# Performance work log

Hardware: AMD Instinct MI355X
Metric: run time of the kernel (lower is better)

## Reference

```python
import jax, jax.numpy as jnp
import numpy as np

N = 12288   # nodes
E = 393216  # edges (avg degree 32)
B = 16      # graphs in batch
F_IN = 15   # node feature dim
H = 32      # hidden_dim
EMB = 64    # embedding_dim
NC = 11     # num_classes
EDIM = 2    # edge feature dim
EPS = 1e-5  # BatchNorm eps


def _bn(x, gamma, beta):
    # training-mode BatchNorm1d: biased batch variance, matches torch normalization
    mu = jnp.mean(x, axis=0)
    var = jnp.var(x, axis=0)
    return gamma * (x - mu) * jax.lax.rsqrt(var + EPS) + beta


def setup_inputs() -> dict:
    key = jax.random.key(0)
    ks = jax.random.split(key, 16)
    def p(k, shape, s=0.05):
        return jax.random.normal(k, shape, dtype=jnp.float32) * s
    z = lambda *s: jnp.zeros(s, jnp.float32)
    o = lambda *s: jnp.ones(s, jnp.float32)
    return {
        "x": jax.random.normal(ks[0], (N, F_IN), dtype=jnp.float32),
        "edge_attr": jax.random.normal(ks[1], (E, EDIM), dtype=jnp.float32),
        "w_edge": p(ks[2], (EDIM, 1)), "b_edge": z(1),
        "w1": p(ks[3], (F_IN, H)), "b1": z(H), "g1": o(H), "be1": z(H),
        "w2": p(ks[4], (H, 2 * H)), "b2": z(2 * H), "g2": o(2 * H), "be2": z(2 * H),
        "w3": p(ks[5], (2 * H, EMB)), "b3": z(EMB), "g3": o(EMB), "be3": z(EMB),
        "wf1": p(ks[6], (EMB, 512)), "bf1": z(512), "gf1": o(512), "bef1": z(512),
        "wf2": p(ks[7], (512, 256)), "bf2": z(256), "gf2": o(256), "bef2": z(256),
        "wf3": p(ks[8], (256, NC)), "bf3": z(NC),
        "edge_index": jax.random.randint(ks[9], (2, E), 0, N, dtype=jnp.int64)
                      if jax.config.jax_enable_x64 else jax.random.randint(ks[9], (2, E), 0, N),
        "batch": jnp.sort(jax.random.randint(ks[10], (N,), 0, B)),
    }


def reference(x, edge_attr, w_edge, b_edge,
              w1, b1, g1, be1, w2, b2, g2, be2, w3, b3, g3, be3,
              wf1, bf1, gf1, bef1, wf2, bf2, gf2, bef2, wf3, bf3,
              edge_index, batch):
    # edge weights: sigmoid(Linear(edge_attr)) -> [E]
    ew = jax.nn.sigmoid(edge_attr @ w_edge + b_edge)[:, 0]
    # dense adjacency with self loops, accumulate duplicates (sparse_coo.to_dense)
    loop = jnp.arange(N)
    row = jnp.concatenate([edge_index[0], loop])
    col = jnp.concatenate([edge_index[1], loop])
    w_aug = jnp.concatenate([ew, jnp.ones((N,), ew.dtype)])
    adj = jnp.zeros((N, N), ew.dtype).at[row, col].add(w_aug)
    # symmetric degree normalization D^-1/2 A D^-1/2
    deg = adj.sum(axis=1)
    dis = jnp.where(deg > 0, jax.lax.rsqrt(jnp.where(deg > 0, deg, 1.0)), 0.0)
    support = dis[:, None] * adj * dis[None, :]
    # three GCN layers: support @ x @ W + b, BN, relu
    h = jax.nn.relu(_bn(support @ x @ w1 + b1, g1, be1))
    h = jax.nn.relu(_bn(support @ h @ w2 + b2, g2, be2))
    h = jax.nn.relu(_bn(support @ h @ w3 + b3, g3, be3))
    # global max pool per graph (empty graphs -> zeros)
    seg = jax.ops.segment_max(h, batch, num_segments=B)
    cnt = jax.ops.segment_sum(jnp.ones((N,), h.dtype), batch, num_segments=B)
    emb = jnp.where(cnt[:, None] > 0, seg, 0.0)
    # MLP head (dropout = identity at inference)
    o = jax.nn.relu(_bn(emb @ wf1 + bf1, gf1, bef1))
    o = jax.nn.relu(_bn(o @ wf2 + bf2, gf2, bef2))
    logits = o @ wf3 + bf3
    return jax.nn.log_softmax(logits, axis=1), emb
```

## Files before the change

### kernel.cpp

```cpp
#include <hip/hip_runtime.h>

#define NN   12288
#define EE   393216
#define WELL 128
#define NELL (NN*WELL)
#define BG   16
#define FIN  15
#define FH1  32
#define FH2  64
#define NCL  11
#define BNEPS 1e-5f
#define NBANK 32

typedef unsigned long long u64;
static inline int cdiv(long a, long b){ return (int)((a + b - 1) / b); }

__device__ __forceinline__ int getIdx(const void* p, long i, int is64){
  return is64 ? (int)((const long long*)p)[i] : ((const int*)p)[i];
}

__device__ __forceinline__ float degOf(unsigned lo){
  return 1.0f + (float)lo * (1.0f/1048576.0f);
}

__global__ void k_pre(u64* deg_cnt, float* csp1, float* csp2, float* csp3,
                      float* embf, const void* ei, const void* batch, int* flags){
  int g = blockIdx.x*256 + threadIdx.x;
  if (g < NN) deg_cnt[g] = 0ull;
  if (g < NBANK*128){ csp1[g] = 0.f; csp2[g] = 0.f; csp3[g] = 0.f; }
  if (g < BG*64) embf[g] = 0.f;
  if (blockIdx.x == 0 && threadIdx.x < 64){
    const int* a = (const int*)ei;
    unsigned long long m0 = __ballot(a[2*threadIdx.x + 1] == 0);
    const int* b = (const int*)batch;
    int j = 96*threadIdx.x;
    unsigned long long m1 = __ballot(b[2*j + 1] == 0);
    if (threadIdx.x == 0){
      flags[0] = (m0 == ~0ull) ? 1 : 0;
      flags[1] = (m1 == ~0ull) ? 1 : 0;
    }
  }
}

__global__ void k_edge(const float* ea, const float* we, const float* bedg,
                       const void* ei, const int* flags, u64* deg_cnt,
                       unsigned* csr_p){
  int e = blockIdx.x*256 + threadIdx.x;
  if (e >= EE) return;
  int is64 = flags[0];
  float2 eav = ((const float2*)ea)[e];
  float z = eav.x*we[0] + eav.y*we[1] + bedg[0];
  float w = 1.0f/(1.0f + expf(-z));
  int r = getIdx(ei, e, is64);
  int c = getIdx(ei, (long)EE + e, is64);
  u64 add = (1ull << 32) | (u64)__float2uint_rn(w * 1048576.0f);
  u64 old = atomicAdd(&deg_cnt[r], add);
  int slot = (int)(old >> 32);
  if (slot < WELL){
    unsigned wfix = __float2uint_rn(w * 131072.0f);
    csr_p[((long)r << 7) + slot] = (unsigned)c | (wfix << 14);
  }
}

__global__ void __launch_bounds__(256) k_fix2(const u64* __restrict__ deg_cnt,
                                              unsigned* __restrict__ csr_p){
  int row = blockIdx.x*4 + (threadIdx.x >> 6);
  int lane = threadIdx.x & 63;
  const unsigned* cl = (const unsigned*)deg_cnt;
  int n = (int)(deg_cnt[row] >> 32);
  n = n < WELL ? n : WELL;
  for (int s = lane; s < n; s += 64){
    long idx = ((long)row << 7) + s;
    unsigned v = csr_p[idx];
    int c = (int)(v & 16383u);
    float w = (float)(v >> 14) * (1.0f/131072.0f);
    w *= rsqrtf(degOf(cl[2*c]));
    csr_p[idx] = (unsigned)c | (__float2uint_rn(w * 131072.0f) << 14);
  }
}

template<int F, int FP, int FO, int APPLY_BN>
__global__ void __launch_bounds__(256) k_layer(
    const float* __restrict__ Hin,
    const float* __restrict__ cspin, const float* __restrict__ gam,
    const float* __restrict__ bet,
    const float* __restrict__ W, const float* __restrict__ bias,
    const u64* __restrict__ deg_cnt, const unsigned* __restrict__ csr_p,
    float* __restrict__ Pout, float* __restrict__ csout){
  const int R2 = 256/(FP*2);
  __shared__ float At[R2][FP];
  __shared__ float Apart[256];
  __shared__ float lcs[FO], lcq[FO];
  __shared__ float lsc[64], lsh[64];
  int tid = threadIdx.x;
  if (tid < FO){ lcs[tid] = 0.f; lcq[tid] = 0.f; }
  if (APPLY_BN && tid < F){
    float s = 0.f, q = 0.f;
    #pragma unroll
    for (int b = 0; b < NBANK; b++){
      s += cspin[b*128 + tid];
      q += cspin[b*128 + 64 + tid];
    }
    float mu  = s*(1.0f/NN);
    float var = q*(1.0f/NN) - mu*mu;
    float sc = gam[tid]*rsqrtf(var + BNEPS);
    lsc[tid] = sc;
    lsh[tid] = bet[tid] - mu*sc;
  }
  __syncthreads();
  int f = tid % FP;
  int sub = tid / FP;
  int kw = sub & 1, lr = sub >> 1;
  float sc = 1.f, sh = 0.f;
  if (APPLY_BN && f < F){ sc = lsc[f]; sh = lsh[f]; }
  int row = blockIdx.x*R2 + lr;
  u64 dc = deg_cnt[row];
  float d = rsqrtf(degOf((unsigned)(dc & 0xffffffffull)));
  int n = (int)(dc >> 32);
  n = n < WELL ? n : WELL;
  float acc = 0.f;
  if (f < F){
    if (kw == 0){
      float v0 = Hin[row*F + f];
      if (APPLY_BN) v0 = fmaxf(v0*sc + sh, 0.f);
      acc = d * v0;
    }
    int nch = (n + 15) >> 4;
    const uint4* pb = (const uint4*)(csr_p + ((long)row << 7));
    for (int ch = kw; ch < nch; ch += 2){
      const uint4* pc = pb + 4*ch;
      uint4 a0 = pc[0], a1 = pc[1], a2 = pc[2], a3 = pc[3];
      unsigned pv[16];
      pv[0]=a0.x; pv[1]=a0.y; pv[2]=a0.z; pv[3]=a0.w;
      pv[4]=a1.x; pv[5]=a1.y; pv[6]=a1.z; pv[7]=a1.w;
      pv[8]=a2.x; pv[9]=a2.y; pv[10]=a2.z; pv[11]=a2.w;
      pv[12]=a3.x; pv[13]=a3.y; pv[14]=a3.z; pv[15]=a3.w;
      int base = ch*16;
      if (base + 16 > n){
        #pragma unroll
        for (int j = 0; j < 16; j++) if (base + j >= n) pv[j] = 0u;
      }
      float hh[16];
      #pragma unroll
      for (int j = 0; j < 16; j++)
        hh[j] = Hin[(int)(pv[j] & 16383u)*F + f];
      #pragma unroll
      for (int j = 0; j < 16; j++){
        float h = hh[j];
        if (APPLY_BN) h = fmaxf(h*sc + sh, 0.f);
        acc += (float)(pv[j] >> 14) * (1.0f/131072.0f) * h;
      }
    }
  }
  Apart[tid] = acc;
  __syncthreads();
  if (f < F && kw == 0)
    At[lr][f] = d * (Apart[tid] + Apart[tid + FP]);
  __syncthreads();
  const int fo = tid % FO;
  float bb = bias[fo];
  for (int o = tid; o < R2*FO; o += 256){
    int l = o / FO;
    float s = bb;
    #pragma unroll
    for (int fi = 0; fi < F; fi++) s += At[l][fi] * W[fi*FO + fo];
    Pout[(blockIdx.x*R2 + l)*FO + fo] = s;
    atomicAdd(&lcs[fo], s);
    atomicAdd(&lcq[fo], s*s);
  }
  __syncthreads();
  if (tid < FO){
    int bank = blockIdx.x & (NBANK-1);
    atomicAdd(&csout[bank*128 + tid],      lcs[tid]);
    atomicAdd(&csout[bank*128 + 64 + tid], lcq[tid]);
  }
}

__global__ void k_pool(const float* P3, const float* csp, const float* gam,
                       const float* bet, const void* batch, const int* flags,
                       float* embf){
  __shared__ float lsc[64], lsh[64];
  if (threadIdx.x < 64){
    float s = 0.f, q = 0.f;
    #pragma unroll
    for (int b = 0; b < NBANK; b++){
      s += csp[b*128 + threadIdx.x];
      q += csp[b*128 + 64 + threadIdx.x];
    }
    float mu  = s*(1.0f/NN);
    float var = q*(1.0f/NN) - mu*mu;
    float sc = gam[threadIdx.x]*rsqrtf(var + BNEPS);
    lsc[threadIdx.x] = sc;
    lsh[threadIdx.x] = bet[threadIdx.x] - mu*sc;
  }
  __syncthreads();
  int is64 = flags[1];
  int b = blockIdx.x & 15, chunk = blockIdx.x >> 4;
  int lo = 0, hi = NN;
  while (lo < hi){ int m = (lo+hi)>>1; if (getIdx(batch, m, is64) < b) lo = m+1; else hi = m; }
  int start = lo;
  lo = start; hi = NN;
  while (lo < hi){ int m = (lo+hi)>>1; if (getIdx(batch, m, is64) < b+1) lo = m+1; else hi = m; }
  int end = lo;
  int f = threadIdx.x & 63, grp = threadIdx.x >> 6;
  float sc = lsc[f], sh = lsh[f];
  float m = 0.0f;
  for (int i = start + chunk*4 + grp; i < end; i += 64)
    m = fmaxf(m, P3[(long)i*FH2 + f]*sc + sh);
  __shared__ float shm[4][64];
  shm[grp][f] = m;
  __syncthreads();
  if (grp == 0){
    float v = fmaxf(fmaxf(shm[0][f], shm[1][f]), fmaxf(shm[2][f], shm[3][f]));
    atomicMax((int*)&embf[b*64 + f], __float_as_int(v));
  }
}

__global__ void __launch_bounds__(256) k_fcA(const float* embf, const float* wf1,
    const float* bf1, const float* gf1, const float* bef1, float* s1g, float* out){
  if (blockIdx.x == 0){
    #pragma unroll
    for (int i = 0; i < 4; i++)
      out[BG*NCL + i*256 + threadIdx.x] = embf[i*256 + threadIdx.x];
  }
  int c = blockIdx.x*4 + (threadIdx.x >> 6);
  int l = threadIdx.x & 63;
  float wcol = wf1[l*512 + c];
  float z[BG];
  #pragma unroll
  for (int r = 0; r < BG; r++){
    float v = embf[r*64 + l] * wcol;
    #pragma unroll
    for (int off = 32; off > 0; off >>= 1) v += __shfl_down(v, off);
    z[r] = v;
  }
  if (l == 0){
    float bb = bf1[c];
    float s = 0.f, q = 0.f;
    #pragma unroll
    for (int r = 0; r < BG; r++){ float zr = z[r] + bb; s += zr; q += zr*zr; }
    float mean = s*(1.f/BG), var = q*(1.f/BG) - mean*mean;
    float inv = rsqrtf(var + BNEPS);
    float gg = gf1[c], b2 = bef1[c];
    #pragma unroll
    for (int r = 0; r < BG; r++)
      s1g[r*512 + c] = fmaxf(gg*(z[r] + bb - mean)*inv + b2, 0.f);
  }
}

__global__ void __launch_bounds__(256) k_fcB(const float* s1g, const float* wf2,
    const float* bf2, const float* gf2, const float* bef2, float* s2g){
  int c = blockIdx.x*4 + (threadIdx.x >> 6);
  int l = threadIdx.x & 63;
  float wreg[8];
  #pragma unroll
  for (int j = 0; j < 8; j++) wreg[j] = wf2[(l + 64*j)*256 + c];
  float z[BG];
  #pragma unroll
  for (int r = 0; r < BG; r++){
    float v = 0.f;
    #pragma unroll
    for (int j = 0; j < 8; j++) v += s1g[r*512 + l + 64*j] * wreg[j];
    #pragma unroll
    for (int off = 32; off > 0; off >>= 1) v += __shfl_down(v, off);
    z[r] = v;
  }
  if (l == 0){
    float bb = bf2[c];
    float s = 0.f, q = 0.f;
    #pragma unroll
    for (int r = 0; r < BG; r++){ float zr = z[r] + bb; s += zr; q += zr*zr; }
    float mean = s*(1.f/BG), var = q*(1.f/BG) - mean*mean;
    float inv = rsqrtf(var + BNEPS);
    float gg = gf2[c], b2 = bef2[c];
    #pragma unroll
    for (int r = 0; r < BG; r++)
      s2g[r*256 + c] = fmaxf(gg*(z[r] + bb - mean)*inv + b2, 0.f);
  }
}

__global__ void k_fc3(const float* s2g, const float* wf3, const float* bf3, float* out){
  __shared__ float s2[BG*256];
  __shared__ float sl[BG*NCL];
  int t = threadIdx.x;
  for (int i = t; i < BG*256; i += 256) s2[i] = s2g[i];
  __syncthreads();
  if (t < BG*NCL){
    int r = t / NCL, c = t - r*NCL;
    float s = bf3[c];
    for (int k = 0; k < 256; k++) s += s2[r*256 + k]*wf3[k*NCL + c];
    sl[t] = s;
  }
  __syncthreads();
  if (t < BG){
    float m = -1e30f;
    for (int c = 0; c < NCL; c++) m = fmaxf(m, sl[t*NCL + c]);
    float s = 0.f;
    for (int c = 0; c < NCL; c++) s += expf(sl[t*NCL + c] - m);
    float lg = logf(s) + m;
    for (int c = 0; c < NCL; c++) out[t*NCL + c] = sl[t*NCL + c] - lg;
  }
}

extern "C" void kernel_launch(void* const* d_in, const int* in_sizes, int n_in,
                              void* d_out, int out_size, void* d_ws, size_t ws_size,
                              hipStream_t stream){
  const float* x    = (const float*)d_in[0];
  const float* ea   = (const float*)d_in[1];
  const float* we   = (const float*)d_in[2];
  const float* bedg = (const float*)d_in[3];
  const float* w1   = (const float*)d_in[4];  const float* b1  = (const float*)d_in[5];
  const float* g1   = (const float*)d_in[6];  const float* be1 = (const float*)d_in[7];
  const float* w2   = (const float*)d_in[8];  const float* b2  = (const float*)d_in[9];
  const float* g2   = (const float*)d_in[10]; const float* be2 = (const float*)d_in[11];
  const float* w3   = (const float*)d_in[12]; const float* b3  = (const float*)d_in[13];
  const float* g3   = (const float*)d_in[14]; const float* be3 = (const float*)d_in[15];
  const float* wf1  = (const float*)d_in[16]; const float* bf1 = (const float*)d_in[17];
  const float* gf1  = (const float*)d_in[18]; const float* bef1= (const float*)d_in[19];
  const float* wf2  = (const float*)d_in[20]; const float* bf2 = (const float*)d_in[21];
  const float* gf2  = (const float*)d_in[22]; const float* bef2= (const float*)d_in[23];
  const float* wf3  = (const float*)d_in[24]; const float* bf3 = (const float*)d_in[25];
  const void* ei    = d_in[26];
  const void* batch = d_in[27];
  float* out = (float*)d_out;

  u64* wq = (u64*)d_ws;
  u64* deg_cnt = wq; wq += NN;
  unsigned* csr_p = (unsigned*)wq; wq += NELL/2;
  float* ws = (float*)wq;
  float* P1    = ws; ws += NN*FH1;
  float* P2    = ws; ws += NN*FH2;
  float* P3    = ws; ws += NN*FH2;
  float* csp1  = ws; ws += NBANK*128;
  float* csp2  = ws; ws += NBANK*128;
  float* csp3  = ws; ws += NBANK*128;
  float* embf  = ws; ws += BG*64;
  float* s1g   = ws; ws += BG*512;
  float* s2g   = ws; ws += BG*256;
  int* flags   = (int*)ws;

  k_pre<<<48, 256, 0, stream>>>(deg_cnt, csp1, csp2, csp3, embf, ei, batch, flags);
  k_edge<<<cdiv(EE,256), 256, 0, stream>>>(ea, we, bedg, ei, flags, deg_cnt, csr_p);
  k_fix2<<<NN/4, 256, 0, stream>>>(deg_cnt, csr_p);

  k_layer<FIN,16,FH1,0><<<NN/8, 256, 0, stream>>>(x, nullptr, nullptr, nullptr,
      w1, b1, deg_cnt, csr_p, P1, csp1);
  k_layer<FH1,32,FH2,1><<<NN/4, 256, 0, stream>>>(P1, csp1, g1, be1,
      w2, b2, deg_cnt, csr_p, P2, csp2);
  k_layer<FH2,64,FH2,1><<<NN/2, 256, 0, stream>>>(P2, csp2, g2, be2,
      w3, b3, deg_cnt, csr_p, P3, csp3);

  k_pool<<<256, 256, 0, stream>>>(P3, csp3, g3, be3, batch, flags, embf);
  k_fcA<<<128, 256, 0, stream>>>(embf, wf1, bf1, gf1, bef1, s1g, out);
  k_fcB<<<64, 256, 0, stream>>>(s1g, wf2, bf2, gf2, bef2, s2g);
  k_fc3<<<1, 256, 0, stream>>>(s2g, wf3, bf3, out);
}
```

Measured before the change: 231.3 us.

## Vectorize GCN layers 2 and 3 gathers with float4 per lane and split-K

Adds a k_layerv kernel for layers 2 and 3. Each lane now gathers four features as one float4 instead of one scalar, and each row's neighbor list is split across KS lane groups whose partial sums are reduced through shared memory. This packs 8 rows per block, cutting the number of threads that re-read the CSR row data and making each gather load wider. Layer 1 keeps the scalar kernel with the BN path stripped out. The trade-offs are more registers per thread (8 float4 gathers in flight) and fewer threads per row overall.

```diff
diff --git a/kernel.cpp b/kernel.cpp
--- a/kernel.cpp
+++ b/kernel.cpp
@@ -79,11 +79,9 @@
   }
 }
 
-template<int F, int FP, int FO, int APPLY_BN>
+template<int F, int FP, int FO>
 __global__ void __launch_bounds__(256) k_layer(
     const float* __restrict__ Hin,
-    const float* __restrict__ cspin, const float* __restrict__ gam,
-    const float* __restrict__ bet,
     const float* __restrict__ W, const float* __restrict__ bias,
     const u64* __restrict__ deg_cnt, const unsigned* __restrict__ csr_p,
     float* __restrict__ Pout, float* __restrict__ csout){
@@ -91,28 +89,11 @@
   __shared__ float At[R2][FP];
   __shared__ float Apart[256];
   __shared__ float lcs[FO], lcq[FO];
-  __shared__ float lsc[64], lsh[64];
   int tid = threadIdx.x;
   if (tid < FO){ lcs[tid] = 0.f; lcq[tid] = 0.f; }
-  if (APPLY_BN && tid < F){
-    float s = 0.f, q = 0.f;
-    #pragma unroll
-    for (int b = 0; b < NBANK; b++){
-      s += cspin[b*128 + tid];
-      q += cspin[b*128 + 64 + tid];
-    }
-    float mu  = s*(1.0f/NN);
-    float var = q*(1.0f/NN) - mu*mu;
-    float sc = gam[tid]*rsqrtf(var + BNEPS);
-    lsc[tid] = sc;
-    lsh[tid] = bet[tid] - mu*sc;
-  }
-  __syncthreads();
   int f = tid % FP;
   int sub = tid / FP;
   int kw = sub & 1, lr = sub >> 1;
-  float sc = 1.f, sh = 0.f;
-  if (APPLY_BN && f < F){ sc = lsc[f]; sh = lsh[f]; }
   int row = blockIdx.x*R2 + lr;
   u64 dc = deg_cnt[row];
   float d = rsqrtf(degOf((unsigned)(dc & 0xffffffffull)));
@@ -120,11 +101,7 @@
   n = n < WELL ? n : WELL;
   float acc = 0.f;
   if (f < F){
-    if (kw == 0){
-      float v0 = Hin[row*F + f];
-      if (APPLY_BN) v0 = fmaxf(v0*sc + sh, 0.f);
-      acc = d * v0;
-    }
+    if (kw == 0) acc = d * Hin[row*F + f];
     int nch = (n + 15) >> 4;
     const uint4* pb = (const uint4*)(csr_p + ((long)row << 7));
     for (int ch = kw; ch < nch; ch += 2){
@@ -145,11 +122,8 @@
       for (int j = 0; j < 16; j++)
         hh[j] = Hin[(int)(pv[j] & 16383u)*F + f];
       #pragma unroll
-      for (int j = 0; j < 16; j++){
-        float h = hh[j];
-        if (APPLY_BN) h = fmaxf(h*sc + sh, 0.f);
-        acc += (float)(pv[j] >> 14) * (1.0f/131072.0f) * h;
-      }
+      for (int j = 0; j < 16; j++)
+        acc += (float)(pv[j] >> 14) * (1.0f/131072.0f) * hh[j];
     }
   }
   Apart[tid] = acc;
@@ -165,6 +139,112 @@
     #pragma unroll
     for (int fi = 0; fi < F; fi++) s += At[l][fi] * W[fi*FO + fo];
     Pout[(blockIdx.x*R2 + l)*FO + fo] = s;
+    atomicAdd(&lcs[fo], s);
+    atomicAdd(&lcq[fo], s*s);
+  }
+  __syncthreads();
+  if (tid < FO){
+    int bank = blockIdx.x & (NBANK-1);
+    atomicAdd(&csout[bank*128 + tid],      lcs[tid]);
+    atomicAdd(&csout[bank*128 + 64 + tid], lcq[tid]);
+  }
+}
+
+template<int F, int LPR, int KS, int FO>
+__global__ void __launch_bounds__(256) k_layerv(
+    const float* __restrict__ Hin,
+    const float* __restrict__ cspin, const float* __restrict__ gam,
+    const float* __restrict__ bet,
+    const float* __restrict__ W, const float* __restrict__ bias,
+    const u64* __restrict__ deg_cnt, const unsigned* __restrict__ csr_p,
+    float* __restrict__ Pout, float* __restrict__ csout){
+  const int R = 256/(LPR*KS);
+  __shared__ float At[R][F];
+  __shared__ float4 Apart[256];
+  __shared__ float lcs[FO], lcq[FO];
+  __shared__ float lsc[64], lsh[64];
+  int tid = threadIdx.x;
+  if (tid < FO){ lcs[tid] = 0.f; lcq[tid] = 0.f; }
+  if (tid < F){
+    float s = 0.f, q = 0.f;
+    #pragma unroll
+    for (int b = 0; b < NBANK; b++){
+      s += cspin[b*128 + tid];
+      q += cspin[b*128 + 64 + tid];
+    }
+    float mu  = s*(1.0f/NN);
+    float var = q*(1.0f/NN) - mu*mu;
+    float sc = gam[tid]*rsqrtf(var + BNEPS);
+    lsc[tid] = sc;
+    lsh[tid] = bet[tid] - mu*sc;
+  }
+  __syncthreads();
+  int fl = tid % LPR;
+  int sub = tid / LPR;
+  int kw = sub % KS, lr = sub / KS;
+  int f0 = fl*4;
+  float sc0 = lsc[f0], sc1 = lsc[f0+1], sc2 = lsc[f0+2], sc3 = lsc[f0+3];
+  float sh0 = lsh[f0], sh1 = lsh[f0+1], sh2 = lsh[f0+2], sh3 = lsh[f0+3];
+  int row = blockIdx.x*R + lr;
+  u64 dc = deg_cnt[row];
+  float d = rsqrtf(degOf((unsigned)(dc & 0xffffffffull)));
+  int n = (int)(dc >> 32);
+  n = n < WELL ? n : WELL;
+  const float4* __restrict__ Hin4 = (const float4*)Hin;
+  float ax = 0.f, ay = 0.f, az = 0.f, aw = 0.f;
+  if (kw == 0){
+    float4 v = Hin4[row*LPR + fl];
+    ax = d * fmaxf(v.x*sc0 + sh0, 0.f);
+    ay = d * fmaxf(v.y*sc1 + sh1, 0.f);
+    az = d * fmaxf(v.z*sc2 + sh2, 0.f);
+    aw = d * fmaxf(v.w*sc3 + sh3, 0.f);
+  }
+  int nch = (n + 7) >> 3;
+  const uint4* pb = (const uint4*)(csr_p + ((long)row << 7));
+  for (int ch = kw; ch < nch; ch += KS){
+    const uint4* pc = pb + 2*ch;
+    uint4 q0 = pc[0], q1 = pc[1];
+    unsigned pv[8];
+    pv[0]=q0.x; pv[1]=q0.y; pv[2]=q0.z; pv[3]=q0.w;
+    pv[4]=q1.x; pv[5]=q1.y; pv[6]=q1.z; pv[7]=q1.w;
+    int base = ch*8;
+    if (base + 8 > n){
+      #pragma unroll
+      for (int j = 0; j < 8; j++) if (base + j >= n) pv[j] = 0u;
+    }
+    float4 h4[8];
+    #pragma unroll
+    for (int j = 0; j < 8; j++)
+      h4[j] = Hin4[(int)(pv[j] & 16383u)*LPR + fl];
+    #pragma unroll
+    for (int j = 0; j < 8; j++){
+      float w = (float)(pv[j] >> 14) * (1.0f/131072.0f);
+      ax += w * fmaxf(h4[j].x*sc0 + sh0, 0.f);
+      ay += w * fmaxf(h4[j].y*sc1 + sh1, 0.f);
+      az += w * fmaxf(h4[j].z*sc2 + sh2, 0.f);
+      aw += w * fmaxf(h4[j].w*sc3 + sh3, 0.f);
+    }
+  }
+  Apart[tid] = make_float4(ax, ay, az, aw);
+  __syncthreads();
+  if (kw == 0){
+    #pragma unroll
+    for (int k = 1; k < KS; k++){
+      float4 p = Apart[tid + k*LPR];
+      ax += p.x; ay += p.y; az += p.z; aw += p.w;
+    }
+    float4* atrow = (float4*)&At[lr][0];
+    atrow[fl] = make_float4(d*ax, d*ay, d*az, d*aw);
+  }
+  __syncthreads();
+  const int fo = tid % FO;
+  float bb = bias[fo];
+  for (int o = tid; o < R*FO; o += 256){
+    int l = o / FO;
+    float s = bb;
+    #pragma unroll
+    for (int fi = 0; fi < F; fi++) s += At[l][fi] * W[fi*FO + fo];
+    Pout[(blockIdx.x*R + l)*FO + fo] = s;
     atomicAdd(&lcs[fo], s);
     atomicAdd(&lcq[fo], s*s);
   }
@@ -343,11 +423,11 @@
   k_edge<<<cdiv(EE,256), 256, 0, stream>>>(ea, we, bedg, ei, flags, deg_cnt, csr_p);
   k_fix2<<<NN/4, 256, 0, stream>>>(deg_cnt, csr_p);
 
-  k_layer<FIN,16,FH1,0><<<NN/8, 256, 0, stream>>>(x, nullptr, nullptr, nullptr,
+  k_layer<FIN,16,FH1><<<NN/8, 256, 0, stream>>>(x,
       w1, b1, deg_cnt, csr_p, P1, csp1);
-  k_layer<FH1,32,FH2,1><<<NN/4, 256, 0, stream>>>(P1, csp1, g1, be1,
+  k_layerv<FH1,8,4,FH2><<<NN/8, 256, 0, stream>>>(P1, csp1, g1, be1,
       w2, b2, deg_cnt, csr_p, P2, csp2);
-  k_layer<FH2,64,FH2,1><<<NN/2, 256, 0, stream>>>(P2, csp2, g2, be2,
+  k_layerv<FH2,16,2,FH2><<<NN/8, 256, 0, stream>>>(P2, csp2, g2, be2,
       w3, b3, deg_cnt, csr_p, P3, csp3);
 
   k_pool<<<256, 256, 0, stream>>>(P3, csp3, g3, be3, batch, flags, embf);
```

New measurement: 223.3 us. 1.04x faster.
